# Kernel optimization log

Measured on AMD Instinct MI355X. Metric: run time of the kernel, lower is better.

## Reference

```python
import jax, jax.numpy as jnp
import numpy as np

N_ENTITIES = 500_000
N_RELS = 1_000
EMB_DIM = 128
N_TRIPLES = 1_000_000

def setup_inputs() -> dict:
    key = jax.random.key(0)
    k1, k2, k3, k4, k5 = jax.random.split(key, 5)
    memory = jax.random.normal(k1, (N_ENTITIES, EMB_DIM), dtype=jnp.float32) * 0.1
    rel_table = jax.random.normal(k2, (N_RELS, EMB_DIM), dtype=jnp.float32)
    h_idx = jax.random.randint(k3, (N_TRIPLES,), 0, N_ENTITIES, dtype=jnp.int32)
    r_idx = jax.random.randint(k4, (N_TRIPLES,), 0, N_RELS, dtype=jnp.int32)
    t_idx = jax.random.randint(k5, (N_TRIPLES,), 0, N_ENTITIES, dtype=jnp.int32)
    return {"memory": memory, "rel_table": rel_table,
            "h_idx": h_idx, "r_idx": r_idx, "t_idx": t_idx}

def reference(memory, rel_table, h_idx, r_idx, t_idx):
    # Gather (all reads use the OLD memory, matching torch: RHS is computed
    # before the index_put).
    h_vec = memory[h_idx]          # [E, D]
    r_vec = rel_table[r_idx]       # [E, D]
    t_vec = memory[t_idx]          # [E, D]
    msg = h_vec + r_vec - t_vec
    new_vals = 0.9 * h_vec + 0.1 * msg   # = h_vec + 0.1*(r_vec - t_vec)
    # matching torch index_put(accumulate=False) semantics.
    return memory.at[h_idx].set(new_vals)
```

## Files before the change

kernel.cpp:

```cpp
#include <hip/hip_runtime.h>

#define N_ENTITIES 500000
#define N_RELS 1000
#define EMB_DIM 128
#define N_TRIPLES 1000000

#define STEPS 4
#define ROWS_PER_STEP 8
#define BLOCK_ROWS (STEPS * ROWS_PER_STEP)

typedef float floatx4 __attribute__((ext_vector_type(4)));
typedef unsigned long long u64;


__global__ void init_pack_kernel(u64* __restrict__ pack) {
    int i = blockIdx.x * blockDim.x + threadIdx.x;
    if (i < N_ENTITIES) pack[i] = 0ull;
}

__global__ void find_winner_kernel(const int4* __restrict__ h4,
                                   const int4* __restrict__ r4,
                                   const int4* __restrict__ t4,
                                   u64* __restrict__ pack) {
    int q = blockIdx.x * blockDim.x + threadIdx.x;
    if (q >= N_TRIPLES / 4) return;
    int4 h = h4[q];
    int4 r = r4[q];
    int4 t = t4[q];
    u64 e1 = (u64)(4 * q + 1);
    atomicMax(&pack[h.x], (e1      << 29) | ((u64)r.x << 19) | (u64)t.x);
    atomicMax(&pack[h.y], ((e1 + 1) << 29) | ((u64)r.y << 19) | (u64)t.y);
    atomicMax(&pack[h.z], ((e1 + 2) << 29) | ((u64)r.z << 19) | (u64)t.z);
    atomicMax(&pack[h.w], ((e1 + 3) << 29) | ((u64)r.w << 19) | (u64)t.w);
}

__global__ void apply_kernel(const float* __restrict__ memory,
                             const float* __restrict__ rel_table,
                             const u64* __restrict__ pack,
                             float* __restrict__ out) {
    int lane = threadIdx.x & 31;
    int hr   = threadIdx.x >> 5;
    int base = blockIdx.x * BLOCK_ROWS;

    int rows[STEPS];
    u64 k[STEPS];
#pragma unroll
    for (int i = 0; i < STEPS; ++i) {
        rows[i] = base + i * ROWS_PER_STEP + hr;
        k[i] = pack[rows[i]];
    }

    floatx4 h[STEPS];
#pragma unroll
    for (int i = 0; i < STEPS; ++i)
        h[i] = ((const floatx4*)(memory + (size_t)rows[i] * EMB_DIM))[lane];

    floatx4 rv[STEPS], tv[STEPS];
#pragma unroll
    for (int i = 0; i < STEPS; ++i) {
        int t = (int)(k[i] & 0x7FFFF);
        int r = (int)((k[i] >> 19) & 0x3FF);
        rv[i] = ((const floatx4*)(rel_table + (size_t)r * EMB_DIM))[lane];
        tv[i] = ((const floatx4*)(memory    + (size_t)t * EMB_DIM))[lane];
    }

#pragma unroll
    for (int i = 0; i < STEPS; ++i) {
        floatx4 upd = 0.9f * h[i] + 0.1f * (h[i] + rv[i] - tv[i]);
        floatx4 val = (k[i] != 0ull) ? upd : h[i];
        floatx4* orow = (floatx4*)(out + (size_t)rows[i] * EMB_DIM) + lane;
        __builtin_nontemporal_store(val, orow);
    }
}

extern "C" void kernel_launch(void* const* d_in, const int* in_sizes, int n_in,
                              void* d_out, int out_size, void* d_ws, size_t ws_size,
                              hipStream_t stream) {
    const float* memory    = (const float*)d_in[0];
    const float* rel_table = (const float*)d_in[1];
    const int*   h_idx     = (const int*)d_in[2];
    const int*   r_idx     = (const int*)d_in[3];
    const int*   t_idx     = (const int*)d_in[4];
    float*       out       = (float*)d_out;

    u64* pack = (u64*)d_ws;

    {
        int threads = 256;
        int blocks = (N_ENTITIES + threads - 1) / threads;
        init_pack_kernel<<<blocks, threads, 0, stream>>>(pack);
    }
    {
        int threads = 256;
        int quads = N_TRIPLES / 4;
        int blocks = (quads + threads - 1) / threads;
        find_winner_kernel<<<blocks, threads, 0, stream>>>(
            (const int4*)h_idx, (const int4*)r_idx, (const int4*)t_idx, pack);
    }
    {
        int threads = 256;
        int blocks = N_ENTITIES / BLOCK_ROWS;
        apply_kernel<<<blocks, threads, 0, stream>>>(memory, rel_table, pack, out);
    }
}
```

Baseline: 483.9 us.

## Replace global 64-bit atomics with LDS segmented winner search and merge-join

Winner selection moves from global 64-bit atomicMax on a random-access pack array to a two-phase scheme. Each block scans one chunk of h_idx and keeps the last triple index per entity, for one entity segment held in LDS. A merge kernel then takes the max over chunks and gathers r/t to build the packed key. This removes scattered global atomics and the separate init pass, but every block re-reads its full index chunk once per segment, and the per-chunk partial arrays cost extra memory traffic. The pack load in the apply kernel also becomes nontemporal, and the old path stays as a fallback when the workspace is too small.

```diff
diff --git a/kernel.cpp b/kernel.cpp
--- a/kernel.cpp
+++ b/kernel.cpp
@@ -4,6 +4,9 @@
 #define N_RELS 1000
 #define EMB_DIM 128
 #define N_TRIPLES 1000000
+
+#define K_SEG 32
+#define SEG (N_ENTITIES / K_SEG)
 
 #define STEPS 4
 #define ROWS_PER_STEP 8
@@ -13,9 +16,59 @@
 typedef unsigned long long u64;
 
 
-__global__ void init_pack_kernel(u64* __restrict__ pack) {
+__global__ void find_seg_kernel(const int* __restrict__ h_idx,
+                                int* __restrict__ partial,
+                                int M, int CH) {
+    __shared__ int lds[SEG];
+    int tid = threadIdx.x;
+    int k = blockIdx.x & (K_SEG - 1);
+    int m = blockIdx.x >> 5;
+
+    for (int i = tid; i < SEG; i += 256) lds[i] = -1;
+    __syncthreads();
+
+    int lo = k * SEG, hi = lo + SEG;
+    const int4* h4 = (const int4*)(h_idx + m * CH);
+    int quads = CH >> 2;
+    for (int q = tid; q < quads; q += 256) {
+        int4 h = h4[q];
+        int e = m * CH + 4 * q;
+        if (h.x >= lo && h.x < hi) atomicMax(&lds[h.x - lo], e);
+        if (h.y >= lo && h.y < hi) atomicMax(&lds[h.y - lo], e + 1);
+        if (h.z >= lo && h.z < hi) atomicMax(&lds[h.z - lo], e + 2);
+        if (h.w >= lo && h.w < hi) atomicMax(&lds[h.w - lo], e + 3);
+    }
+    __syncthreads();
+
+    int* slice = partial + (size_t)(m * K_SEG + k) * SEG;
+    for (int i = tid; i < SEG; i += 256) slice[i] = lds[i];
+}
+
+__global__ void merge_join_kernel(const int* __restrict__ partial,
+                                  const int* __restrict__ r_idx,
+                                  const int* __restrict__ t_idx,
+                                  u64* __restrict__ pack,
+                                  int M) {
+    int v = blockIdx.x * blockDim.x + threadIdx.x;
+    if (v >= N_ENTITIES) return;
+    int k = v / SEG, i = v - k * SEG;
+    int w = -1;
+    for (int m = 0; m < M; ++m) {
+        int cand = partial[(size_t)(m * K_SEG + k) * SEG + i];
+        w = (cand > w) ? cand : w;
+    }
+    u64 key = 0ull;
+    if (w >= 0) {
+        u64 r = (u64)(unsigned)r_idx[w];
+        u64 t = (u64)(unsigned)t_idx[w];
+        key = ((u64)(w + 1) << 29) | (r << 19) | t;
+    }
+    pack[v] = key;
+}
+
+__global__ void init_pack_kernel(ulonglong2* __restrict__ pack2, int n2) {
     int i = blockIdx.x * blockDim.x + threadIdx.x;
-    if (i < N_ENTITIES) pack[i] = 0ull;
+    if (i < n2) { ulonglong2 z; z.x = 0ull; z.y = 0ull; pack2[i] = z; }
 }
 
 __global__ void find_winner_kernel(const int4* __restrict__ h4,
@@ -24,9 +77,7 @@
                                    u64* __restrict__ pack) {
     int q = blockIdx.x * blockDim.x + threadIdx.x;
     if (q >= N_TRIPLES / 4) return;
-    int4 h = h4[q];
-    int4 r = r4[q];
-    int4 t = t4[q];
+    int4 h = h4[q]; int4 r = r4[q]; int4 t = t4[q];
     u64 e1 = (u64)(4 * q + 1);
     atomicMax(&pack[h.x], (e1      << 29) | ((u64)r.x << 19) | (u64)t.x);
     atomicMax(&pack[h.y], ((e1 + 1) << 29) | ((u64)r.y << 19) | (u64)t.y);
@@ -47,7 +98,7 @@
 #pragma unroll
     for (int i = 0; i < STEPS; ++i) {
         rows[i] = base + i * ROWS_PER_STEP + hr;
-        k[i] = pack[rows[i]];
+        k[i] = __builtin_nontemporal_load(&pack[rows[i]]);
     }
 
     floatx4 h[STEPS];
@@ -83,23 +134,32 @@
     const int*   t_idx     = (const int*)d_in[4];
     float*       out       = (float*)d_out;
 
-    u64* pack = (u64*)d_ws;
+    size_t pack_bytes = (size_t)N_ENTITIES * sizeof(u64);
 
-    {
-        int threads = 256;
-        int blocks = (N_ENTITIES + threads - 1) / threads;
-        init_pack_kernel<<<blocks, threads, 0, stream>>>(pack);
-    }
-    {
-        int threads = 256;
-        int quads = N_TRIPLES / 4;
-        int blocks = (quads + threads - 1) / threads;
-        find_winner_kernel<<<blocks, threads, 0, stream>>>(
+    int M = 0;
+    if      (ws_size >= 16 * (size_t)N_ENTITIES * 4 + pack_bytes) M = 16;
+    else if (ws_size >=  8 * (size_t)N_ENTITIES * 4 + pack_bytes) M = 8;
+    else if (ws_size >=  4 * (size_t)N_ENTITIES * 4 + pack_bytes) M = 4;
+
+    if (M > 0) {
+        int* partial = (int*)d_ws;
+        u64* pack = (u64*)((char*)d_ws + (size_t)M * N_ENTITIES * 4);
+        int CH = N_TRIPLES / M;
+        find_seg_kernel<<<K_SEG * M, 256, 0, stream>>>(h_idx, partial, M, CH);
+        merge_join_kernel<<<(N_ENTITIES + 255) / 256, 256, 0, stream>>>(
+            partial, r_idx, t_idx, pack, M);
+        apply_kernel<<<N_ENTITIES / BLOCK_ROWS, 256, 0, stream>>>(
+            memory, rel_table, pack, out);
+    } else {
+        u64* pack = (u64*)d_ws;
+        {
+            int n2 = N_ENTITIES / 2;
+            init_pack_kernel<<<(n2 + 255) / 256, 256, 0, stream>>>(
+                (ulonglong2*)pack, n2);
+        }
+        find_winner_kernel<<<(N_TRIPLES / 4 + 255) / 256, 256, 0, stream>>>(
             (const int4*)h_idx, (const int4*)r_idx, (const int4*)t_idx, pack);
-    }
-    {
-        int threads = 256;
-        int blocks = N_ENTITIES / BLOCK_ROWS;
-        apply_kernel<<<blocks, threads, 0, stream>>>(memory, rel_table, pack, out);
+        apply_kernel<<<N_ENTITIES / BLOCK_ROWS, 256, 0, stream>>>(
+            memory, rel_table, pack, out);
     }
 }
```

Result: slower. 494.5 us (+2.2%).

## Replace global atomic winner search with per-segment LDS atomics and fused init

Applied to the files above, without the earlier changes.

Drops the separate init kernel and the global 64-bit atomicMax scatter. Instead 250 blocks each own a 2000-entity segment, scan all h indices, and pick the last writer with shared-memory atomicMax. Each block then writes its packed keys directly, which removes global atomic contention and the zero-fill pass. In exchange, every block rereads the full 4 MB h_idx array (about 1 GB of L2 traffic in total), and only 250 blocks run, which may underfill the GPU. The pack load in the apply kernel also becomes nontemporal.

```diff
diff --git a/kernel.cpp b/kernel.cpp
--- a/kernel.cpp
+++ b/kernel.cpp
@@ -4,6 +4,10 @@
 #define N_RELS 1000
 #define EMB_DIM 128
 #define N_TRIPLES 1000000
+
+#define N_SEG_BLOCKS 250
+#define SEG_ENT (N_ENTITIES / N_SEG_BLOCKS)
+#define FIND_THREADS 1024
 
 #define STEPS 4
 #define ROWS_PER_STEP 8
@@ -13,25 +17,40 @@
 typedef unsigned long long u64;
 
 
-__global__ void init_pack_kernel(u64* __restrict__ pack) {
-    int i = blockIdx.x * blockDim.x + threadIdx.x;
-    if (i < N_ENTITIES) pack[i] = 0ull;
-}
+__global__ __launch_bounds__(FIND_THREADS)
+void find_pack_kernel(const int4* __restrict__ h4,
+                      const int* __restrict__ r_idx,
+                      const int* __restrict__ t_idx,
+                      u64* __restrict__ pack) {
+    __shared__ int best[SEG_ENT];
+    int tid = threadIdx.x;
+    int lo  = blockIdx.x * SEG_ENT;
 
-__global__ void find_winner_kernel(const int4* __restrict__ h4,
-                                   const int4* __restrict__ r4,
-                                   const int4* __restrict__ t4,
-                                   u64* __restrict__ pack) {
-    int q = blockIdx.x * blockDim.x + threadIdx.x;
-    if (q >= N_TRIPLES / 4) return;
-    int4 h = h4[q];
-    int4 r = r4[q];
-    int4 t = t4[q];
-    u64 e1 = (u64)(4 * q + 1);
-    atomicMax(&pack[h.x], (e1      << 29) | ((u64)r.x << 19) | (u64)t.x);
-    atomicMax(&pack[h.y], ((e1 + 1) << 29) | ((u64)r.y << 19) | (u64)t.y);
-    atomicMax(&pack[h.z], ((e1 + 2) << 29) | ((u64)r.z << 19) | (u64)t.z);
-    atomicMax(&pack[h.w], ((e1 + 3) << 29) | ((u64)r.w << 19) | (u64)t.w);
+    for (int i = tid; i < SEG_ENT; i += FIND_THREADS) best[i] = -1;
+    __syncthreads();
+
+    const int QUADS = N_TRIPLES / 4;
+    for (int q = tid; q < QUADS; q += FIND_THREADS) {
+        int4 h = h4[q];
+        int e = 4 * q;
+        unsigned a;
+        a = (unsigned)(h.x - lo); if (a < (unsigned)SEG_ENT) atomicMax(&best[a], e);
+        a = (unsigned)(h.y - lo); if (a < (unsigned)SEG_ENT) atomicMax(&best[a], e + 1);
+        a = (unsigned)(h.z - lo); if (a < (unsigned)SEG_ENT) atomicMax(&best[a], e + 2);
+        a = (unsigned)(h.w - lo); if (a < (unsigned)SEG_ENT) atomicMax(&best[a], e + 3);
+    }
+    __syncthreads();
+
+    for (int i = tid; i < SEG_ENT; i += FIND_THREADS) {
+        int w = best[i];
+        u64 key = 0ull;
+        if (w >= 0) {
+            u64 r = (u64)(unsigned)r_idx[w];
+            u64 t = (u64)(unsigned)t_idx[w];
+            key = ((u64)(w + 1) << 29) | (r << 19) | t;
+        }
+        pack[lo + i] = key;
+    }
 }
 
 __global__ void apply_kernel(const float* __restrict__ memory,
@@ -47,7 +66,7 @@
 #pragma unroll
     for (int i = 0; i < STEPS; ++i) {
         rows[i] = base + i * ROWS_PER_STEP + hr;
-        k[i] = pack[rows[i]];
+        k[i] = __builtin_nontemporal_load(&pack[rows[i]]);
     }
 
     floatx4 h[STEPS];
@@ -85,21 +104,9 @@
 
     u64* pack = (u64*)d_ws;
 
-    {
-        int threads = 256;
-        int blocks = (N_ENTITIES + threads - 1) / threads;
-        init_pack_kernel<<<blocks, threads, 0, stream>>>(pack);
-    }
-    {
-        int threads = 256;
-        int quads = N_TRIPLES / 4;
-        int blocks = (quads + threads - 1) / threads;
-        find_winner_kernel<<<blocks, threads, 0, stream>>>(
-            (const int4*)h_idx, (const int4*)r_idx, (const int4*)t_idx, pack);
-    }
-    {
-        int threads = 256;
-        int blocks = N_ENTITIES / BLOCK_ROWS;
-        apply_kernel<<<blocks, threads, 0, stream>>>(memory, rel_table, pack, out);
-    }
+    find_pack_kernel<<<N_SEG_BLOCKS, FIND_THREADS, 0, stream>>>(
+        (const int4*)h_idx, r_idx, t_idx, pack);
+
+    apply_kernel<<<N_ENTITIES / BLOCK_ROWS, 256, 0, stream>>>(
+        memory, rel_table, pack, out);
 }
```

New measurement: 571.8 us. +18.2%, slower.
